# Kernel optimization log

Measured on AMD Instinct MI355X. Metric: run time of the kernel, lower is better.

The kernel has to match this reference:

```python
import jax, jax.numpy as jnp
import numpy as np

B, S, D, M = 4, 1024, 128, 20000
THRESH = 0.1          # memory.query_with_indices threshold
CW_MIN = 0.01         # compound_weight > 0.01 gate
TI_MIN = 0.01         # total_influence > 0.01 gate
NORM_EPS = 1e-6       # norm_sq > 1e-6 gate
INF_EPS = 1e-5        # division epsilon


def setup_inputs() -> dict:
    key = jax.random.key(0)
    ks = jax.random.split(key, 4)
    sd = 1.0 / np.sqrt(D)
    return {
        "input_tensor": jax.random.normal(ks[0], (B, S, D), dtype=jnp.float32),
        "mem": jax.random.normal(ks[1], (M, D), dtype=jnp.float32),
        "W1": jax.random.normal(ks[2], (D, D), dtype=jnp.float32) * sd,
        "b1": jnp.zeros((D,), dtype=jnp.float32),
        "ln_g": jnp.ones((D,), dtype=jnp.float32),
        "ln_b": jnp.zeros((D,), dtype=jnp.float32),
        "W2": jax.random.normal(ks[3], (D, D), dtype=jnp.float32) * sd,
        "b2": jnp.zeros((D,), dtype=jnp.float32),
    }


def reference(input_tensor, mem, W1, b1, ln_g, ln_b, W2, b2):
    x = input_tensor  # [B,S,D]
    # fusion_net: Linear -> LayerNorm -> ReLU
    h = jnp.einsum("bsd,ed->bse", x, W1) + b1
    mu = h.mean(-1, keepdims=True)
    var = h.var(-1, keepdims=True)
    h = (h - mu) * jax.lax.rsqrt(var + 1e-5) * ln_g + ln_b
    feats = jax.nn.relu(h)
    raw = jnp.einsum("bsd,ed->bse", feats, W2) + b2  # [B,S,D]

    # GraphMemory query: cosine similarity, keep entries with sim > THRESH
    xn = x * jax.lax.rsqrt(jnp.sum(x * x, -1, keepdims=True) + 1e-12)
    mn = mem * jax.lax.rsqrt(jnp.sum(mem * mem, -1, keepdims=True) + 1e-12)
    sim = jnp.einsum("bsd,md->bsm", xn, mn)              # [B,S,M]
    w = jnp.where(sim > THRESH, sim, 0.0)                # per-token weights

    # compound_weight per batch & memory slot (sum over seq positions)
    cw = w.sum(axis=1)                                   # [B,M]
    norm_sq = jnp.sum(mem * mem, -1)                     # [M]
    active = (cw > CW_MIN) & (norm_sq > NORM_EPS)        # [B,M]
    eff = jnp.where(active, cw, 0.0)                     # effective weights

    # projection of each target vec onto each memory vec
    safe_ns = jnp.where(norm_sq > NORM_EPS, norm_sq, 1.0)
    coef = jnp.einsum("bsd,md->bsm", raw, mem) / safe_ns # [B,S,M]
    correction = jnp.einsum("bsm,bm,md->bsd", coef, eff, mem)  # [B,S,D]

    ti = eff.sum(-1)                                     # [B] total_influence
    corr = correction / (ti + INF_EPS)[:, None, None]
    final = jnp.where((ti > TI_MIN)[:, None, None], raw + 0.5 * corr, raw)
    return final
```

## Files before the change

kernel.cpp:

```cpp
#include <hip/hip_runtime.h>

#define DD 128
#define SS 1024
#define BB 4
#define M_TOT 20000
#define M_PAD 20480
#define GM_NCH 64
#define GM_CH 320
#define FMLP_BLOCKS 128
#define PREP_BLOCKS 320

typedef __bf16 bf16x8 __attribute__((ext_vector_type(8)));
typedef _Float16 f16x8 __attribute__((ext_vector_type(8)));
typedef unsigned short u16x8 __attribute__((ext_vector_type(8)));
typedef float f32x16 __attribute__((ext_vector_type(16)));

union BF8 { bf16x8 b; u16x8 u; };

__device__ __forceinline__ unsigned short f2bf(float f) {
    __bf16 h = (__bf16)f;
    return __builtin_bit_cast(unsigned short, h);
}
__device__ __forceinline__ float bf2f(unsigned short h) {
    return __uint_as_float(((unsigned int)h) << 16);
}

__global__ __launch_bounds__(256) void k_front(
    const float* __restrict__ x, const float* __restrict__ W1,
    const float* __restrict__ b1, const float* __restrict__ ln_g,
    const float* __restrict__ ln_b, const float* __restrict__ W2,
    const float* __restrict__ b2, const float* __restrict__ mem,
    unsigned short* __restrict__ xnb, float* __restrict__ raw,
    unsigned short* __restrict__ mnb, _Float16* __restrict__ mnT,
    float* __restrict__ norm_sq, float* __restrict__ ti,
    float* __restrict__ cw) {
    __shared__ __align__(16) char smem_raw[64 * 136 * 2];
    const int tid = threadIdx.x;
    const int bid = blockIdx.x;

    if (bid < FMLP_BLOCKS) {
        unsigned short* featsL = (unsigned short*)smem_raw;
        float* redp = (float*)(smem_raw + 8704);
        float2* stats = (float2*)(smem_raw + 8704 + 1024);
        const int lane = tid & 63, wv = tid >> 6;
        const int col = lane & 31, hi = lane >> 5;
        const int t0 = bid * 32;
        const int ct = wv;

        bf16x8 Af[8];
        float sq = 0.f;
        const float* xrow = x + (size_t)(t0 + col) * DD + hi * 8;
        #pragma unroll
        for (int kk = 0; kk < 8; ++kk) {
            float4 p = *(const float4*)(xrow + kk * 16);
            float4 q = *(const float4*)(xrow + kk * 16 + 4);
            BF8 t;
            t.u[0] = f2bf(p.x); t.u[1] = f2bf(p.y); t.u[2] = f2bf(p.z); t.u[3] = f2bf(p.w);
            t.u[4] = f2bf(q.x); t.u[5] = f2bf(q.y); t.u[6] = f2bf(q.z); t.u[7] = f2bf(q.w);
            Af[kk] = t.b;
            sq += p.x * p.x + p.y * p.y + p.z * p.z + p.w * p.w;
            sq += q.x * q.x + q.y * q.y + q.z * q.z + q.w * q.w;
        }
        sq += __shfl_xor(sq, 32);
        float xrs = rsqrtf(sq + 1e-12f);
        if (wv == 0) {
            unsigned short* xo = xnb + (size_t)(t0 + col) * DD + hi * 8;
            #pragma unroll
            for (int kk = 0; kk < 8; ++kk) {
                BF8 t; t.b = Af[kk];
                u16x8 o;
                #pragma unroll
                for (int j = 0; j < 8; ++j) o[j] = f2bf(bf2f(t.u[j]) * xrs);
                *(u16x8*)(xo + kk * 16) = o;
            }
        }

        f32x16 acc;
        {
            float bv = b1[ct * 32 + col];
            #pragma unroll
            for (int r = 0; r < 16; ++r) acc[r] = bv;
        }
        const float* w1row = W1 + (size_t)(ct * 32 + col) * DD + hi * 8;
        #pragma unroll
        for (int kk = 0; kk < 8; ++kk) {
            float4 p = *(const float4*)(w1row + kk * 16);
            float4 q = *(const float4*)(w1row + kk * 16 + 4);
            BF8 t;
            t.u[0] = f2bf(p.x); t.u[1] = f2bf(p.y); t.u[2] = f2bf(p.z); t.u[3] = f2bf(p.w);
            t.u[4] = f2bf(q.x); t.u[5] = f2bf(q.y); t.u[6] = f2bf(q.z); t.u[7] = f2bf(q.w);
            acc = __builtin_amdgcn_mfma_f32_32x32x16_bf16(Af[kk], t.b, acc, 0, 0, 0);
        }

        float rs_[16], rq_[16];
        #pragma unroll
        for (int r = 0; r < 16; ++r) { float v = acc[r]; rs_[r] = v; rq_[r] = v * v; }
        #pragma unroll
        for (int off = 1; off < 32; off <<= 1) {
            #pragma unroll
            for (int r = 0; r < 16; ++r) {
                rs_[r] += __shfl_xor(rs_[r], off);
                rq_[r] += __shfl_xor(rq_[r], off);
            }
        }
        if (col == 0) {
            #pragma unroll
            for (int r = 0; r < 16; ++r) {
                int row = (r & 3) + 8 * (r >> 2) + 4 * hi;
                redp[(wv * 32 + row) * 2 + 0] = rs_[r];
                redp[(wv * 32 + row) * 2 + 1] = rq_[r];
            }
        }
        __syncthreads();
        if (tid < 32) {
            float S = redp[(0 * 32 + tid) * 2] + redp[(1 * 32 + tid) * 2] +
                      redp[(2 * 32 + tid) * 2] + redp[(3 * 32 + tid) * 2];
            float Q = redp[(0 * 32 + tid) * 2 + 1] + redp[(1 * 32 + tid) * 2 + 1] +
                      redp[(2 * 32 + tid) * 2 + 1] + redp[(3 * 32 + tid) * 2 + 1];
            float mu = S * (1.f / 128.f);
            float rstd = rsqrtf(Q * (1.f / 128.f) - mu * mu + 1e-5f);
            stats[tid] = make_float2(mu, rstd);
        }
        __syncthreads();

        {
            float gv = ln_g[ct * 32 + col], bv = ln_b[ct * 32 + col];
            #pragma unroll
            for (int r = 0; r < 16; ++r) {
                int row = (r & 3) + 8 * (r >> 2) + 4 * hi;
                float2 st = stats[row];
                float v = fmaxf((acc[r] - st.x) * st.y * gv + bv, 0.f);
                featsL[row * 136 + ct * 32 + col] = f2bf(v);
            }
        }
        __syncthreads();

        f32x16 a2;
        {
            float bv = b2[ct * 32 + col];
            #pragma unroll
            for (int r = 0; r < 16; ++r) a2[r] = bv;
        }
        const float* w2row = W2 + (size_t)(ct * 32 + col) * DD + hi * 8;
        #pragma unroll
        for (int kk = 0; kk < 8; ++kk) {
            bf16x8 Aq = *(const bf16x8*)&featsL[(lane & 31) * 136 + hi * 8 + kk * 16];
            float4 p = *(const float4*)(w2row + kk * 16);
            float4 q = *(const float4*)(w2row + kk * 16 + 4);
            BF8 t;
            t.u[0] = f2bf(p.x); t.u[1] = f2bf(p.y); t.u[2] = f2bf(p.z); t.u[3] = f2bf(p.w);
            t.u[4] = f2bf(q.x); t.u[5] = f2bf(q.y); t.u[6] = f2bf(q.z); t.u[7] = f2bf(q.w);
            a2 = __builtin_amdgcn_mfma_f32_32x32x16_bf16(Aq, t.b, a2, 0, 0, 0);
        }
        #pragma unroll
        for (int r = 0; r < 16; ++r) {
            int row = (r & 3) + 8 * (r >> 2) + 4 * hi;
            raw[(size_t)(t0 + row) * DD + ct * 32 + col] = a2[r];
        }
    } else {
        unsigned short* RM = (unsigned short*)smem_raw;
        const int pb = bid - FMLP_BLOCKS;
        const int m0 = pb * 64;
        cw[pb * 256 + tid] = 0.0f;
        if (pb == 0 && tid < BB) ti[tid] = 0.0f;

        const int r = tid >> 2, seg = tid & 3;
        const int m = m0 + r;
        const bool ok = m < M_TOT;
        float4 v[8];
        const float4* src = (const float4*)mem + (size_t)m * 32 + seg * 8;
        #pragma unroll
        for (int i = 0; i < 8; ++i)
            v[i] = ok ? src[i] : make_float4(0.f, 0.f, 0.f, 0.f);
        float ss = 0.f;
        #pragma unroll
        for (int i = 0; i < 8; ++i)
            ss += v[i].x * v[i].x + v[i].y * v[i].y + v[i].z * v[i].z + v[i].w * v[i].w;
        ss += __shfl_xor(ss, 1);
        ss += __shfl_xor(ss, 2);
        float rs = rsqrtf(ss + 1e-12f);
        if (seg == 0) norm_sq[m] = ss;

        #pragma unroll
        for (int i = 0; i < 4; ++i) {
            float4 a = v[2 * i], bq = v[2 * i + 1];
            u16x8 o;
            o[0] = f2bf(a.x * rs); o[1] = f2bf(a.y * rs);
            o[2] = f2bf(a.z * rs); o[3] = f2bf(a.w * rs);
            o[4] = f2bf(bq.x * rs); o[5] = f2bf(bq.y * rs);
            o[6] = f2bf(bq.z * rs); o[7] = f2bf(bq.w * rs);
            *(u16x8*)(mnb + (size_t)m * DD + seg * 32 + i * 8) = o;
            *(u16x8*)(RM + r * 136 + seg * 32 + i * 8) = o;
        }
        __syncthreads();
        const int d = tid >> 1, half = tid & 1;
        _Float16* dst = mnT + (size_t)d * M_PAD + m0 + half * 32;
        #pragma unroll
        for (int q = 0; q < 4; ++q) {
            f16x8 o;
            #pragma unroll
            for (int j = 0; j < 8; ++j)
                o[j] = (_Float16)bf2f(RM[(half * 32 + q * 8 + j) * 136 + d]);
            *(f16x8*)(dst + q * 8) = o;
        }
    }
}

__global__ __launch_bounds__(256, 3) void k_cw(
    const unsigned short* __restrict__ xnb, const unsigned short* __restrict__ mnb,
    float* __restrict__ cw) {
    __shared__ unsigned short As[4][32 * 128];
    const int tid = threadIdx.x, lane = tid & 63, wv = tid >> 6;
    const int c = lane & 31, h = lane >> 5;
    const int b = blockIdx.z;
    const int mw = blockIdx.x * 256 + wv * 64;
    const int s_base = blockIdx.y * 256;

    const int srow = tid >> 4, sk16 = tid & 15;
    const int soff = srow * 128 + ((sk16 * 8) ^ ((srow & 15) << 3));
    const int srow1 = srow + 16;
    const int soff1 = srow1 * 128 + ((sk16 * 8) ^ ((srow1 & 15) << 3));
    const unsigned short* xbase = xnb + ((size_t)b * SS + s_base) * DD;

    bf16x8 Bf[2][8];
    #pragma unroll
    for (int ct = 0; ct < 2; ++ct)
        #pragma unroll
        for (int kk = 0; kk < 8; ++kk)
            Bf[ct][kk] = *(const bf16x8*)(mnb + (size_t)(mw + ct * 32 + c) * DD +
                                          kk * 16 + h * 8);

    {
        u16x8 a0 = *(const u16x8*)(xbase + (size_t)srow * DD + sk16 * 8);
        u16x8 a1 = *(const u16x8*)(xbase + (size_t)srow1 * DD + sk16 * 8);
        const unsigned short* n1 = xbase + (size_t)32 * DD;
        u16x8 b0 = *(const u16x8*)(n1 + (size_t)srow * DD + sk16 * 8);
        u16x8 b1 = *(const u16x8*)(n1 + (size_t)srow1 * DD + sk16 * 8);
        *(u16x8*)&As[0][soff] = a0; *(u16x8*)&As[0][soff1] = a1;
        *(u16x8*)&As[1][soff] = b0; *(u16x8*)&As[1][soff1] = b1;
    }

    float cw0 = 0.f, cw1 = 0.f;
    #pragma unroll 1
    for (int p = 0; p < 4; ++p) {
        __syncthreads();
        u16x8 w0, w1, w2, w3;
        if (p < 3) {
            const unsigned short* n0 = xbase + (size_t)(2 * p + 2) * 32 * DD;
            const unsigned short* n1 = xbase + (size_t)(2 * p + 3) * 32 * DD;
            w0 = *(const u16x8*)(n0 + (size_t)srow * DD + sk16 * 8);
            w1 = *(const u16x8*)(n0 + (size_t)srow1 * DD + sk16 * 8);
            w2 = *(const u16x8*)(n1 + (size_t)srow * DD + sk16 * 8);
            w3 = *(const u16x8*)(n1 + (size_t)srow1 * DD + sk16 * 8);
        }
        {
            f32x16 p0, p1;
            #pragma unroll
            for (int r = 0; r < 16; ++r) { p0[r] = 0.f; p1[r] = 0.f; }
            const unsigned short* Ab = As[(2 * p) & 3];
            __builtin_amdgcn_s_setprio(1);
            #pragma unroll
            for (int kk = 0; kk < 8; ++kk) {
                bf16x8 Afr = *(const bf16x8*)&Ab[c * 128 + ((kk * 16 + h * 8) ^ ((c & 15) << 3))];
                p0 = __builtin_amdgcn_mfma_f32_32x32x16_bf16(Afr, Bf[0][kk], p0, 0, 0, 0);
                p1 = __builtin_amdgcn_mfma_f32_32x32x16_bf16(Afr, Bf[1][kk], p1, 0, 0, 0);
            }
            __builtin_amdgcn_s_setprio(0);
            #pragma unroll
            for (int r = 0; r < 16; ++r) {
                float a = p0[r], bb = p1[r];
                cw0 += a > 0.1f ? a : 0.f;
                cw1 += bb > 0.1f ? bb : 0.f;
            }
        }
        {
            f32x16 p0, p1;
            #pragma unroll
            for (int r = 0; r < 16; ++r) { p0[r] = 0.f; p1[r] = 0.f; }
            const unsigned short* Ab = As[(2 * p + 1) & 3];
            __builtin_amdgcn_s_setprio(1);
            #pragma unroll
            for (int kk = 0; kk < 8; ++kk) {
                bf16x8 Afr = *(const bf16x8*)&Ab[c * 128 + ((kk * 16 + h * 8) ^ ((c & 15) << 3))];
                p0 = __builtin_amdgcn_mfma_f32_32x32x16_bf16(Afr, Bf[0][kk], p0, 0, 0, 0);
                p1 = __builtin_amdgcn_mfma_f32_32x32x16_bf16(Afr, Bf[1][kk], p1, 0, 0, 0);
            }
            __builtin_amdgcn_s_setprio(0);
            if (p < 3) {
                unsigned short* An0 = As[(2 * p + 2) & 3];
                unsigned short* An1 = As[(2 * p + 3) & 3];
                *(u16x8*)&An0[soff] = w0; *(u16x8*)&An0[soff1] = w1;
                *(u16x8*)&An1[soff] = w2; *(u16x8*)&An1[soff1] = w3;
            }
            #pragma unroll
            for (int r = 0; r < 16; ++r) {
                float a = p0[r], bb = p1[r];
                cw0 += a > 0.1f ? a : 0.f;
                cw1 += bb > 0.1f ? bb : 0.f;
            }
        }
    }
    cw0 += __shfl_xor(cw0, 32);
    cw1 += __shfl_xor(cw1, 32);
    if (lane < 32) {
        atomicAdd(&cw[(size_t)b * M_PAD + mw + c], cw0);
        atomicAdd(&cw[(size_t)b * M_PAD + mw + 32 + c], cw1);
    }
}

__global__ __launch_bounds__(256) void k_gmatm(
    const _Float16* __restrict__ mnT, const float* __restrict__ cw,
    const float* __restrict__ norm_sq, float* __restrict__ ti,
    float* __restrict__ pG) {
    __shared__ __align__(16) _Float16 effH[GM_CH];
    __shared__ float rb[4];
    const int tid = threadIdx.x, lane = tid & 63, wv = tid >> 6;
    const int c = lane & 31, h = lane >> 5;
    const int b = blockIdx.y;
    const int m0 = blockIdx.x * GM_CH;

    float tsum = 0.f;
    #pragma unroll
    for (int idx = tid; idx < GM_CH; idx += 256) {
        int m = m0 + idx;
        float e = 0.f;
        if (m < M_TOT) {
            float cc = cw[(size_t)b * M_PAD + m];
            float ns = norm_sq[m];
            e = (cc > 0.01f && ns > 1e-6f) ? cc : 0.f;
        }
        effH[idx] = (_Float16)e;
        tsum += e;
    }
    #pragma unroll
    for (int off = 1; off < 64; off <<= 1) tsum += __shfl_xor(tsum, off);
    if (lane == 0) rb[wv] = tsum;
    __syncthreads();
    if (tid == 0) atomicAdd(&ti[b], rb[0] + rb[1] + rb[2] + rb[3]);

    f32x16 a0, a1, a2, a3;
    #pragma unroll
    for (int r = 0; r < 16; ++r) { a0[r] = 0.f; a1[r] = 0.f; a2[r] = 0.f; a3[r] = 0.f; }

    const _Float16* Arow = mnT + (size_t)(wv * 32 + c) * M_PAD + m0;
    const _Float16* B0r = mnT + (size_t)(0 * 32 + c) * M_PAD + m0;
    const _Float16* B1r = mnT + (size_t)(1 * 32 + c) * M_PAD + m0;
    const _Float16* B2r = mnT + (size_t)(2 * 32 + c) * M_PAD + m0;
    const _Float16* B3r = mnT + (size_t)(3 * 32 + c) * M_PAD + m0;

    #pragma unroll 1
    for (int t = 0; t < GM_CH / 64; ++t) {
        #pragma unroll
        for (int kk = 0; kk < 4; ++kk) {
            const int mo = t * 64 + kk * 16 + h * 8;
            f16x8 au = *(const f16x8*)(Arow + mo);
            f16x8 ef = *(const f16x8*)&effH[mo];
            f16x8 af = au * ef;
            f16x8 B0 = *(const f16x8*)(B0r + mo);
            f16x8 B1 = *(const f16x8*)(B1r + mo);
            f16x8 B2 = *(const f16x8*)(B2r + mo);
            f16x8 B3 = *(const f16x8*)(B3r + mo);
            a0 = __builtin_amdgcn_mfma_f32_32x32x16_f16(af, B0, a0, 0, 0, 0);
            a1 = __builtin_amdgcn_mfma_f32_32x32x16_f16(af, B1, a1, 0, 0, 0);
            a2 = __builtin_amdgcn_mfma_f32_32x32x16_f16(af, B2, a2, 0, 0, 0);
            a3 = __builtin_amdgcn_mfma_f32_32x32x16_f16(af, B3, a3, 0, 0, 0);
        }
    }
    float* o = pG + (size_t)(blockIdx.x * BB + b) * (DD * DD);
    #pragma unroll
    for (int r = 0; r < 16; ++r) {
        int rf = (r & 3) + 8 * (r >> 2) + 4 * h;
        o[(wv * 32 + rf) * DD + 0 * 32 + c] = a0[r];
        o[(wv * 32 + rf) * DD + 1 * 32 + c] = a1[r];
        o[(wv * 32 + rf) * DD + 2 * 32 + c] = a2[r];
        o[(wv * 32 + rf) * DD + 3 * 32 + c] = a3[r];
    }
}

__global__ __launch_bounds__(256) void k_gmat2(const float* __restrict__ pG,
                                               unsigned short* __restrict__ Gb) {
    __shared__ float4 redv[256];
    const int tid = threadIdx.x;
    const int b = blockIdx.y;
    const int f4i = blockIdx.x * 64 + (tid & 63);
    const int cg = tid >> 6;
    const float4* pG4 = (const float4*)pG;
    float4 s = make_float4(0.f, 0.f, 0.f, 0.f);
    for (int c = cg; c < GM_NCH; c += 4) {
        float4 p = pG4[(size_t)(c * BB + b) * (DD * DD / 4) + f4i];
        s.x += p.x; s.y += p.y; s.z += p.z; s.w += p.w;
    }
    redv[tid] = s;
    __syncthreads();
    if (tid < 64) {
        float4 r0 = redv[tid], r1 = redv[tid + 64], r2 = redv[tid + 128], r3 = redv[tid + 192];
        ushort4 o;
        o.x = f2bf(r0.x + r1.x + r2.x + r3.x);
        o.y = f2bf(r0.y + r1.y + r2.y + r3.y);
        o.z = f2bf(r0.z + r1.z + r2.z + r3.z);
        o.w = f2bf(r0.w + r1.w + r2.w + r3.w);
        *(ushort4*)&Gb[(size_t)b * (DD * DD) + f4i * 4] = o;
    }
}

__global__ __launch_bounds__(256) void k_final(
    const float* __restrict__ raw, const unsigned short* __restrict__ Gb,
    const float* __restrict__ ti, float* __restrict__ out) {
    const int tid = threadIdx.x, lane = tid & 63, wv = tid >> 6;
    const int col = lane & 31, hi = lane >> 5;
    const int t0 = blockIdx.x * 32;
    const int b = blockIdx.x >> 5;
    const int ct = wv;

    bf16x8 Af[8];
    const float* rrow = raw + (size_t)(t0 + col) * DD + hi * 8;
    #pragma unroll
    for (int kk = 0; kk < 8; ++kk) {
        float4 p = *(const float4*)(rrow + kk * 16);
        float4 q = *(const float4*)(rrow + kk * 16 + 4);
        BF8 t;
        t.u[0] = f2bf(p.x); t.u[1] = f2bf(p.y); t.u[2] = f2bf(p.z); t.u[3] = f2bf(p.w);
        t.u[4] = f2bf(q.x); t.u[5] = f2bf(q.y); t.u[6] = f2bf(q.z); t.u[7] = f2bf(q.w);
        Af[kk] = t.b;
    }
    f32x16 acc;
    #pragma unroll
    for (int r = 0; r < 16; ++r) acc[r] = 0.f;
    const unsigned short* grow = Gb + (size_t)b * DD * DD + (size_t)(ct * 32 + col) * DD + hi * 8;
    #pragma unroll
    for (int kk = 0; kk < 8; ++kk) {
        bf16x8 Bw = *(const bf16x8*)(grow + kk * 16);
        acc = __builtin_amdgcn_mfma_f32_32x32x16_bf16(Af[kk], Bw, acc, 0, 0, 0);
    }
    float tib = ti[b];
    float scale = (tib > 0.01f) ? 0.5f / (tib + 1e-5f) : 0.0f;
    #pragma unroll
    for (int r = 0; r < 16; ++r) {
        int row = (r & 3) + 8 * (r >> 2) + 4 * hi;
        size_t idx = (size_t)(t0 + row) * DD + ct * 32 + col;
        out[idx] = raw[idx] + scale * acc[r];
    }
}

extern "C" void kernel_launch(void* const* d_in, const int* in_sizes, int n_in,
                              void* d_out, int out_size, void* d_ws, size_t ws_size,
                              hipStream_t stream) {
    const float* x   = (const float*)d_in[0];
    const float* mem = (const float*)d_in[1];
    const float* W1  = (const float*)d_in[2];
    const float* b1  = (const float*)d_in[3];
    const float* lg  = (const float*)d_in[4];
    const float* lb  = (const float*)d_in[5];
    const float* W2  = (const float*)d_in[6];
    const float* b2  = (const float*)d_in[7];
    float* out = (float*)d_out;

    float* wsf = (float*)d_ws;
    size_t off = 0;
    unsigned short* mnb = (unsigned short*)(wsf + off); off += (size_t)M_PAD * 64;
    _Float16* mnT = (_Float16*)(wsf + off);             off += (size_t)M_PAD * 64;
    float* norm_sq = wsf + off;                         off += M_PAD;
    unsigned short* xnb = (unsigned short*)(wsf + off); off += (size_t)BB * SS * 64;
    float* raw = wsf + off;                             off += (size_t)BB * SS * DD;
    float* cw  = wsf + off;                             off += (size_t)BB * M_PAD;
    unsigned short* Gb = (unsigned short*)(wsf + off);  off += (size_t)BB * DD * DD / 2;
    float* ti  = wsf + off;                             off += BB;
    float* pG  = wsf + off;                             off += (size_t)GM_NCH * BB * DD * DD;

    k_front<<<dim3(FMLP_BLOCKS + PREP_BLOCKS), 256, 0, stream>>>(
        x, W1, b1, lg, lb, W2, b2, mem, xnb, raw, mnb, mnT, norm_sq, ti, cw);
    k_cw<<<dim3(M_PAD / 256, 4, BB), 256, 0, stream>>>(xnb, mnb, cw);
    k_gmatm<<<dim3(GM_NCH, BB), 256, 0, stream>>>(mnT, cw, norm_sq, ti, pG);
    k_gmat2<<<dim3(DD * DD / 256, BB), 256, 0, stream>>>(pG, Gb);
    k_final<<<dim3(SS * BB / 32), 256, 0, stream>>>(raw, Gb, ti, out);
}
```

Before: 77.23 us.

## Halve partial-G traffic with fp16, split prep and final grids, retune k_cw

Stores the per-chunk partial Gram matrices as fp16 instead of fp32 and reduces them with 8-wide loads, halving the write and read traffic between k_gmatm and k_gmat2. The memory-prep part of k_front now uses twice as many blocks, each handling 32 rows. k_final is split across a second grid dimension with 128-thread blocks. k_cw raises its occupancy hint to 4 and splits its prefetch of the next x tiles so fewer registers are live at once. The fp16 partials lose some precision and range in the accumulation, and the extra blocks add scheduling work.

```diff
diff --git a/kernel.cpp b/kernel.cpp
--- a/kernel.cpp
+++ b/kernel.cpp
@@ -8,7 +8,7 @@
 #define GM_NCH 64
 #define GM_CH 320
 #define FMLP_BLOCKS 128
-#define PREP_BLOCKS 320
+#define PREP_BLOCKS 640
 
 typedef __bf16 bf16x8 __attribute__((ext_vector_type(8)));
 typedef _Float16 f16x8 __attribute__((ext_vector_type(8)));
@@ -160,53 +160,54 @@
     } else {
         unsigned short* RM = (unsigned short*)smem_raw;
         const int pb = bid - FMLP_BLOCKS;
-        const int m0 = pb * 64;
-        cw[pb * 256 + tid] = 0.0f;
+        const int m0 = pb * 32;
+        if (pb < BB * M_PAD / 256) cw[pb * 256 + tid] = 0.0f;
         if (pb == 0 && tid < BB) ti[tid] = 0.0f;
 
-        const int r = tid >> 2, seg = tid & 3;
+        const int r = tid >> 3, seg = tid & 7;
         const int m = m0 + r;
         const bool ok = m < M_TOT;
-        float4 v[8];
-        const float4* src = (const float4*)mem + (size_t)m * 32 + seg * 8;
-        #pragma unroll
-        for (int i = 0; i < 8; ++i)
+        float4 v[4];
+        const float4* src = (const float4*)mem + (size_t)m * 32 + seg * 4;
+        #pragma unroll
+        for (int i = 0; i < 4; ++i)
             v[i] = ok ? src[i] : make_float4(0.f, 0.f, 0.f, 0.f);
         float ss = 0.f;
         #pragma unroll
-        for (int i = 0; i < 8; ++i)
+        for (int i = 0; i < 4; ++i)
             ss += v[i].x * v[i].x + v[i].y * v[i].y + v[i].z * v[i].z + v[i].w * v[i].w;
         ss += __shfl_xor(ss, 1);
         ss += __shfl_xor(ss, 2);
+        ss += __shfl_xor(ss, 4);
         float rs = rsqrtf(ss + 1e-12f);
         if (seg == 0) norm_sq[m] = ss;
 
         #pragma unroll
-        for (int i = 0; i < 4; ++i) {
+        for (int i = 0; i < 2; ++i) {
             float4 a = v[2 * i], bq = v[2 * i + 1];
             u16x8 o;
             o[0] = f2bf(a.x * rs); o[1] = f2bf(a.y * rs);
             o[2] = f2bf(a.z * rs); o[3] = f2bf(a.w * rs);
             o[4] = f2bf(bq.x * rs); o[5] = f2bf(bq.y * rs);
             o[6] = f2bf(bq.z * rs); o[7] = f2bf(bq.w * rs);
-            *(u16x8*)(mnb + (size_t)m * DD + seg * 32 + i * 8) = o;
-            *(u16x8*)(RM + r * 136 + seg * 32 + i * 8) = o;
+            *(u16x8*)(mnb + (size_t)m * DD + seg * 16 + i * 8) = o;
+            *(u16x8*)(RM + r * 136 + seg * 16 + i * 8) = o;
         }
         __syncthreads();
         const int d = tid >> 1, half = tid & 1;
-        _Float16* dst = mnT + (size_t)d * M_PAD + m0 + half * 32;
-        #pragma unroll
-        for (int q = 0; q < 4; ++q) {
+        _Float16* dst = mnT + (size_t)d * M_PAD + m0 + half * 16;
+        #pragma unroll
+        for (int q = 0; q < 2; ++q) {
             f16x8 o;
             #pragma unroll
             for (int j = 0; j < 8; ++j)
-                o[j] = (_Float16)bf2f(RM[(half * 32 + q * 8 + j) * 136 + d]);
+                o[j] = (_Float16)bf2f(RM[(half * 16 + q * 8 + j) * 136 + d]);
             *(f16x8*)(dst + q * 8) = o;
         }
     }
 }
 
-__global__ __launch_bounds__(256, 3) void k_cw(
+__global__ __launch_bounds__(256, 4) void k_cw(
     const unsigned short* __restrict__ xnb, const unsigned short* __restrict__ mnb,
     float* __restrict__ cw) {
     __shared__ unsigned short As[4][32 * 128];
@@ -244,14 +245,11 @@
     #pragma unroll 1
     for (int p = 0; p < 4; ++p) {
         __syncthreads();
-        u16x8 w0, w1, w2, w3;
+        u16x8 w0, w1;
         if (p < 3) {
             const unsigned short* n0 = xbase + (size_t)(2 * p + 2) * 32 * DD;
-            const unsigned short* n1 = xbase + (size_t)(2 * p + 3) * 32 * DD;
             w0 = *(const u16x8*)(n0 + (size_t)srow * DD + sk16 * 8);
             w1 = *(const u16x8*)(n0 + (size_t)srow1 * DD + sk16 * 8);
-            w2 = *(const u16x8*)(n1 + (size_t)srow * DD + sk16 * 8);
-            w3 = *(const u16x8*)(n1 + (size_t)srow1 * DD + sk16 * 8);
         }
         {
             f32x16 p0, p1;
@@ -272,6 +270,12 @@
                 cw0 += a > 0.1f ? a : 0.f;
                 cw1 += bb > 0.1f ? bb : 0.f;
             }
+        }
+        u16x8 w2, w3;
+        if (p < 3) {
+            const unsigned short* n1 = xbase + (size_t)(2 * p + 3) * 32 * DD;
+            w2 = *(const u16x8*)(n1 + (size_t)srow * DD + sk16 * 8);
+            w3 = *(const u16x8*)(n1 + (size_t)srow1 * DD + sk16 * 8);
         }
         {
             f32x16 p0, p1;
@@ -311,7 +315,7 @@
 __global__ __launch_bounds__(256) void k_gmatm(
     const _Float16* __restrict__ mnT, const float* __restrict__ cw,
     const float* __restrict__ norm_sq, float* __restrict__ ti,
-    float* __restrict__ pG) {
+    _Float16* __restrict__ pG) {
     __shared__ __align__(16) _Float16 effH[GM_CH];
     __shared__ float rb[4];
     const int tid = threadIdx.x, lane = tid & 63, wv = tid >> 6;
@@ -366,51 +370,50 @@
             a3 = __builtin_amdgcn_mfma_f32_32x32x16_f16(af, B3, a3, 0, 0, 0);
         }
     }
-    float* o = pG + (size_t)(blockIdx.x * BB + b) * (DD * DD);
+    _Float16* o = pG + (size_t)(blockIdx.x * BB + b) * (DD * DD);
     #pragma unroll
     for (int r = 0; r < 16; ++r) {
         int rf = (r & 3) + 8 * (r >> 2) + 4 * h;
-        o[(wv * 32 + rf) * DD + 0 * 32 + c] = a0[r];
-        o[(wv * 32 + rf) * DD + 1 * 32 + c] = a1[r];
-        o[(wv * 32 + rf) * DD + 2 * 32 + c] = a2[r];
-        o[(wv * 32 + rf) * DD + 3 * 32 + c] = a3[r];
-    }
-}
-
-__global__ __launch_bounds__(256) void k_gmat2(const float* __restrict__ pG,
+        o[(wv * 32 + rf) * DD + 0 * 32 + c] = (_Float16)a0[r];
+        o[(wv * 32 + rf) * DD + 1 * 32 + c] = (_Float16)a1[r];
+        o[(wv * 32 + rf) * DD + 2 * 32 + c] = (_Float16)a2[r];
+        o[(wv * 32 + rf) * DD + 3 * 32 + c] = (_Float16)a3[r];
+    }
+}
+
+__global__ __launch_bounds__(256) void k_gmat2(const _Float16* __restrict__ pG,
                                                unsigned short* __restrict__ Gb) {
-    __shared__ float4 redv[256];
+    __shared__ float red[4][64][8];
     const int tid = threadIdx.x;
     const int b = blockIdx.y;
-    const int f4i = blockIdx.x * 64 + (tid & 63);
-    const int cg = tid >> 6;
-    const float4* pG4 = (const float4*)pG;
-    float4 s = make_float4(0.f, 0.f, 0.f, 0.f);
+    const int sl = tid & 63, cg = tid >> 6;
+    const int f8i = blockIdx.x * 64 + sl;
+    float acc[8] = {0.f, 0.f, 0.f, 0.f, 0.f, 0.f, 0.f, 0.f};
     for (int c = cg; c < GM_NCH; c += 4) {
-        float4 p = pG4[(size_t)(c * BB + b) * (DD * DD / 4) + f4i];
-        s.x += p.x; s.y += p.y; s.z += p.z; s.w += p.w;
-    }
-    redv[tid] = s;
+        f16x8 p = *(const f16x8*)(pG + (size_t)(c * BB + b) * (DD * DD) + (size_t)f8i * 8);
+        #pragma unroll
+        for (int j = 0; j < 8; ++j) acc[j] += (float)p[j];
+    }
+    #pragma unroll
+    for (int j = 0; j < 8; ++j) red[cg][sl][j] = acc[j];
     __syncthreads();
     if (tid < 64) {
-        float4 r0 = redv[tid], r1 = redv[tid + 64], r2 = redv[tid + 128], r3 = redv[tid + 192];
-        ushort4 o;
-        o.x = f2bf(r0.x + r1.x + r2.x + r3.x);
-        o.y = f2bf(r0.y + r1.y + r2.y + r3.y);
-        o.z = f2bf(r0.z + r1.z + r2.z + r3.z);
-        o.w = f2bf(r0.w + r1.w + r2.w + r3.w);
-        *(ushort4*)&Gb[(size_t)b * (DD * DD) + f4i * 4] = o;
-    }
-}
-
-__global__ __launch_bounds__(256) void k_final(
+        u16x8 o;
+        #pragma unroll
+        for (int j = 0; j < 8; ++j)
+            o[j] = f2bf(red[0][tid][j] + red[1][tid][j] + red[2][tid][j] + red[3][tid][j]);
+        *(u16x8*)&Gb[(size_t)b * DD * DD + (size_t)(blockIdx.x * 64 + tid) * 8] = o;
+    }
+}
+
+__global__ __launch_bounds__(128) void k_final(
     const float* __restrict__ raw, const unsigned short* __restrict__ Gb,
     const float* __restrict__ ti, float* __restrict__ out) {
     const int tid = threadIdx.x, lane = tid & 63, wv = tid >> 6;
     const int col = lane & 31, hi = lane >> 5;
     const int t0 = blockIdx.x * 32;
     const int b = blockIdx.x >> 5;
-    const int ct = wv;
+    const int ct = blockIdx.y * 2 + wv;
 
     bf16x8 Af[8];
     const float* rrow = raw + (size_t)(t0 + col) * DD + hi * 8;
@@ -465,12 +468,12 @@
     float* cw  = wsf + off;                             off += (size_t)BB * M_PAD;
     unsigned short* Gb = (unsigned short*)(wsf + off);  off += (size_t)BB * DD * DD / 2;
     float* ti  = wsf + off;                             off += BB;
-    float* pG  = wsf + off;                             off += (size_t)GM_NCH * BB * DD * DD;
+    _Float16* pG = (_Float16*)(wsf + off);              off += (size_t)GM_NCH * BB * DD * DD / 2;
 
     k_front<<<dim3(FMLP_BLOCKS + PREP_BLOCKS), 256, 0, stream>>>(
         x, W1, b1, lg, lb, W2, b2, mem, xnb, raw, mnb, mnT, norm_sq, ti, cw);
     k_cw<<<dim3(M_PAD / 256, 4, BB), 256, 0, stream>>>(xnb, mnb, cw);
     k_gmatm<<<dim3(GM_NCH, BB), 256, 0, stream>>>(mnT, cw, norm_sq, ti, pG);
-    k_gmat2<<<dim3(DD * DD / 256, BB), 256, 0, stream>>>(pG, Gb);
-    k_final<<<dim3(SS * BB / 32), 256, 0, stream>>>(raw, Gb, ti, out);
-}
+    k_gmat2<<<dim3(DD * DD / 512, BB), 256, 0, stream>>>(pG, Gb);
+    k_final<<<dim3(SS * BB / 32, 2), 128, 0, stream>>>(raw, Gb, ti, out);
+}
```

After: 122.5 us. +58.6%, slower.
